# Kernel tuning notes

Hardware: AMD Instinct MI355X
Metric: run time of the kernel (lower is better)

The kernel has to match this reference:

```python
import jax, jax.numpy as jnp
import numpy as np

B, L, D_FEAT = 16, 2048, 512
H, D_HID, UNITS = 8, 512, 512


def setup_inputs() -> dict:
    key = jax.random.key(0)
    ks = jax.random.split(key, 8)
    s_feat = 1.0 / np.sqrt(D_FEAT)
    s_hid = 1.0 / np.sqrt(D_HID)
    s_u = 1.0 / np.sqrt(UNITS)
    return {
        "features": jax.random.normal(ks[0], (B, L, D_FEAT), jnp.float32),
        "hidden": jax.random.normal(ks[1], (B, H, D_HID), jnp.float32),
        # Per-head Dense params stacked along a leading head axis.
        "W1": jax.random.normal(ks[2], (H, D_FEAT, UNITS), jnp.float32) * s_feat,
        "b1": jnp.zeros((H, UNITS), jnp.float32),
        "W2": jax.random.normal(ks[3], (H, D_HID, UNITS), jnp.float32) * s_hid,
        "b2": jnp.zeros((H, UNITS), jnp.float32),
        "V": jax.random.normal(ks[4], (H, UNITS), jnp.float32) * s_u,
        "bV": jnp.zeros((H,), jnp.float32),
    }


def reference(features, hidden, W1, b1, W2, b2, V, bV):
    # features: [B, L, Df]; hidden: [B, H, Dh]
    # Per-head: tanh(W1(features) + W2(hidden_h)) -> V -> softmax over L -> weighted sum.
    f_proj = jnp.einsum("bld,hdu->bhlu", features, W1) + b1[None, :, None, :]   # [B,H,L,U]
    h_proj = jnp.einsum("bhd,hdu->bhu", hidden, W2) + b2[None, :, :]            # [B,H,U]
    act = jnp.tanh(f_proj + h_proj[:, :, None, :])                               # [B,H,L,U]
    score = jnp.einsum("bhlu,hu->bhl", act, V) + bV[None, :, None]               # [B,H,L]
    attn = jax.nn.softmax(score, axis=-1)                                        # softmax over L
    context = jnp.einsum("bhl,bld->bhd", attn, features)                         # [B,H,Df]
    # Original stacks weights (each [B,L,1]) along axis=2 -> [B,L,H,1]
    attention_weights = jnp.transpose(attn, (0, 2, 1))[..., None]                # [B,L,H,1]
    return context, attention_weights
```

## Files before the change

kernel.cpp:

```cpp
#include <hip/hip_runtime.h>
#include <hip/hip_bf16.h>

#define B_ 16
#define L_ 2048
#define DF 512
#define H_ 8
#define DH 512
#define U_ 512

typedef unsigned short u16;
typedef __attribute__((ext_vector_type(8))) short bf16x8;
typedef __attribute__((ext_vector_type(4))) float f32x4;

__device__ __forceinline__ u16 f2bf(float x) {
  __hip_bfloat16 h = __float2bfloat16(x);
  u16 u;
  __builtin_memcpy(&u, &h, 2);
  return u;
}

__device__ __forceinline__ float bf2f(u16 u) {
  unsigned x = ((unsigned)u) << 16;
  float f;
  __builtin_memcpy(&f, &x, 4);
  return f;
}

__device__ __forceinline__ void load_lds16(const void* g, void* l) {
  __builtin_amdgcn_global_load_lds(
      (const __attribute__((address_space(1))) void*)g,
      (__attribute__((address_space(3))) void*)l, 16, 0, 0);
}

__device__ __forceinline__ float fast_tanh2(float x) {
  float e = __expf(2.f * x);
  return 1.f - __fdividef(2.f, e + 1.f);
}

__global__ __launch_bounds__(256) void prep_kernel(
    const float* __restrict__ F, u16* __restrict__ Abf,
    const float* __restrict__ W1, u16* __restrict__ W1T,
    const float* __restrict__ hidden, const float* __restrict__ W2,
    float* __restrict__ hpart) {
  __shared__ float t[32][33];
  __shared__ float hs[B_][64];
  if (blockIdx.x < 16384) {
    size_t i = ((size_t)blockIdx.x * 256 + threadIdx.x) * 4;
    float4 v = *(const float4*)(F + i);
    ushort4 o;
    o.x = f2bf(v.x); o.y = f2bf(v.y); o.z = f2bf(v.z); o.w = f2bf(v.w);
    *(ushort4*)(Abf + i) = o;
  } else if (blockIdx.x < 18432) {
    int bid = blockIdx.x - 16384;
    int d0 = (bid & 15) * 32, u0 = ((bid >> 4) & 15) * 32, h = bid >> 8;
    const float* src = W1 + (size_t)h * DF * U_;
    u16* dst = W1T + (size_t)h * U_ * DF;
#pragma unroll
    for (int i = 0; i < 4; ++i) {
      int idx = threadIdx.x + i * 256;
      int r = idx >> 5, c = idx & 31;
      t[r][c] = src[(size_t)(d0 + r) * U_ + u0 + c];
    }
    __syncthreads();
#pragma unroll
    for (int i = 0; i < 4; ++i) {
      int idx = threadIdx.x + i * 256;
      int r = idx >> 5, c = idx & 31;
      dst[(size_t)(u0 + r) * DF + d0 + c] = f2bf(t[c][r]);
    }
  } else {
    int bid = blockIdx.x - 18432;
    int h = bid & 7, uy = (bid >> 3) & 1, dz = bid >> 4;
    int u = uy * 256 + threadIdx.x;
    int d0 = dz * 64;
    for (int idx = threadIdx.x; idx < B_ * 64; idx += 256) {
      int b = idx >> 6, d = idx & 63;
      hs[b][d] = hidden[(size_t)(b * H_ + h) * DH + d0 + d];
    }
    __syncthreads();
    float acc[B_];
#pragma unroll
    for (int b = 0; b < B_; b++) acc[b] = 0.f;
    const float* w2p = W2 + ((size_t)h * DH + d0) * U_ + u;
    for (int d = 0; d < 64; d++) {
      float w = w2p[(size_t)d * U_];
#pragma unroll
      for (int b = 0; b < B_; b++) acc[b] += hs[b][d] * w;
    }
#pragma unroll
    for (int b = 0; b < B_; b++)
      hpart[(((size_t)dz * B_ + b) * H_ + h) * U_ + u] = acc[b];
  }
}

__global__ __launch_bounds__(256) void hproj_combine_kernel(
    const float* __restrict__ partial, const float* __restrict__ b1,
    const float* __restrict__ b2, float* __restrict__ c) {
  int i = blockIdx.x * 256 + threadIdx.x;
  int hu = i & (H_ * U_ - 1);
  float s = b1[hu] + b2[hu];
#pragma unroll
  for (int z = 0; z < 8; z++) s += partial[(size_t)z * B_ * H_ * U_ + i];
  c[i] = s;
}

#define BKV 64

__global__ __launch_bounds__(1024, 4) void score_kernel(
    const u16* __restrict__ Abf, const u16* __restrict__ W1T,
    const float* __restrict__ C, const float* __restrict__ V,
    float* __restrict__ score) {
  int l0 = blockIdx.x * 256;
  int b = blockIdx.y, h = blockIdx.z;
  int tid = threadIdx.x;
  int lane = tid & 63, wid = tid >> 6;
  int wr = wid >> 2, wc = wid & 3;
  int rl = lane & 15, q = lane >> 4;
  int khalf = q << 3;

  __shared__ u16 As[2][256 * BKV];
  __shared__ u16 Bs[2][256 * BKV];
  __shared__ float redsm[4][256];

  const u16* Fb = Abf + ((size_t)b * L_ + l0) * DF;
  const u16* Wh = W1T + (size_t)h * U_ * DF;
  const float* Cb = C + (size_t)(b * H_ + h) * U_;
  const float* Vh = V + (size_t)h * U_;

  float cu[2][4], vv[2][4];
#pragma unroll
  for (int nc = 0; nc < 2; ++nc)
#pragma unroll
    for (int n = 0; n < 4; ++n) {
      int col = nc * 256 + wc * 64 + n * 16 + rl;
      cu[nc][n] = Cb[col];
      vv[nc][n] = Vh[col];
    }

  float part[16];
#pragma unroll
  for (int p = 0; p < 16; ++p) part[p] = 0.f;

  f32x4 acc[4][4];
#pragma unroll
  for (int m = 0; m < 4; ++m)
#pragma unroll
    for (int n = 0; n < 4; ++n)
#pragma unroll
      for (int j = 0; j < 4; ++j) acc[m][n][j] = cu[0][n];

#define STAGE(buf, kb, N0)                                                 \
  {                                                                        \
    _Pragma("unroll") for (int i_ = 0; i_ < 2; ++i_) {                     \
      int idx_ = i_ * 1024 + tid;                                          \
      int row_ = idx_ >> 3;                                                \
      int ke_ = ((idx_ & 7) ^ (row_ & 7)) << 3;                            \
      load_lds16(Fb + ((size_t)row_ << 9) + (kb) + ke_,                    \
                 &As[buf][idx_ * 8]);                                      \
      load_lds16(Wh + (((size_t)((N0) + row_)) << 9) + (kb) + ke_,         \
                 &Bs[buf][idx_ * 8]);                                      \
    }                                                                      \
  }

#define COMPUTE(bufi)                                                      \
  {                                                                        \
    _Pragma("unroll") for (int ss = 0; ss < 2; ++ss) {                     \
      bf16x8 bF[4];                                                        \
      _Pragma("unroll") for (int n = 0; n < 4; ++n) {                      \
        int rB = wc * 64 + n * 16 + rl;                                    \
        bF[n] = *(const bf16x8*)&Bs[bufi][(rB << 6) +                      \
                                          ((ss * 32 + khalf) ^             \
                                           ((rB & 7) << 3))];              \
      }                                                                    \
      _Pragma("unroll") for (int m = 0; m < 4; ++m) {                      \
        int rA = wr * 64 + m * 16 + rl;                                    \
        bf16x8 aF = *(const bf16x8*)&As[bufi][(rA << 6) +                  \
                                             ((ss * 32 + khalf) ^          \
                                              ((rA & 7) << 3))];           \
        _Pragma("unroll") for (int n = 0; n < 4; ++n)                      \
          acc[m][n] = __builtin_amdgcn_mfma_f32_16x16x32_bf16(             \
              aF, bF[n], acc[m][n], 0, 0, 0);                              \
      }                                                                    \
    }                                                                      \
  }

  STAGE(0, 0, 0);

#pragma unroll 1
  for (int s = 0; s < 16; ++s) {
    int cur = s & 1;
    if (s < 15) {
      int kb = ((s + 1) & 7) * BKV;
      int N0n = ((s + 1) >> 3) * 256;
      STAGE(cur ^ 1, kb, N0n);
      asm volatile("s_waitcnt vmcnt(4)" ::: "memory");
    } else {
      asm volatile("s_waitcnt vmcnt(0)" ::: "memory");
    }
    __builtin_amdgcn_s_barrier();
    COMPUTE(cur);
    if (s == 7) {
#pragma unroll
      for (int n = 0; n < 4; ++n)
#pragma unroll
        for (int m = 0; m < 4; ++m)
#pragma unroll
          for (int j = 0; j < 4; ++j) {
            part[m * 4 + j] += fast_tanh2(acc[m][n][j]) * vv[0][n];
            acc[m][n][j] = cu[1][n];
          }
    }
    asm volatile("s_waitcnt lgkmcnt(0)" ::: "memory");
    __builtin_amdgcn_s_barrier();
  }
#pragma unroll
  for (int n = 0; n < 4; ++n)
#pragma unroll
    for (int m = 0; m < 4; ++m)
#pragma unroll
      for (int j = 0; j < 4; ++j)
        part[m * 4 + j] += fast_tanh2(acc[m][n][j]) * vv[1][n];
#undef STAGE
#undef COMPUTE

#pragma unroll
  for (int p = 0; p < 16; ++p) {
    float v = part[p];
    v += __shfl_xor(v, 1, 64);
    v += __shfl_xor(v, 2, 64);
    v += __shfl_xor(v, 4, 64);
    v += __shfl_xor(v, 8, 64);
    part[p] = v;
  }
  __syncthreads();
  if (rl == 0) {
#pragma unroll
    for (int m = 0; m < 4; ++m)
#pragma unroll
      for (int j = 0; j < 4; ++j)
        redsm[wc][wr * 64 + m * 16 + q * 4 + j] = part[m * 4 + j];
  }
  __syncthreads();
  if (tid < 256) {
    float s = redsm[0][tid] + redsm[1][tid] + redsm[2][tid] + redsm[3][tid];
    score[(size_t)(b * H_ + h) * L_ + l0 + tid] = s;
  }
}

__global__ __launch_bounds__(256) void softmax_kernel(
    const float* __restrict__ score, float* __restrict__ attn,
    float* __restrict__ aw_out) {
  int bh = blockIdx.x;
  int b = bh / H_, h = bh % H_;
  const float* s = score + (size_t)bh * L_;
  __shared__ float sv[L_];
  __shared__ float red[256];

  for (int i = threadIdx.x; i < L_ / 4; i += 256)
    ((float4*)sv)[i] = ((const float4*)s)[i];
  __syncthreads();

  float m = -1e30f;
  for (int l = threadIdx.x; l < L_; l += 256) m = fmaxf(m, sv[l]);
  red[threadIdx.x] = m;
  __syncthreads();
  for (int st = 128; st > 0; st >>= 1) {
    if (threadIdx.x < st)
      red[threadIdx.x] = fmaxf(red[threadIdx.x], red[threadIdx.x + st]);
    __syncthreads();
  }
  m = red[0];
  __syncthreads();

  float sum = 0.f;
  for (int l = threadIdx.x; l < L_; l += 256) sum += __expf(sv[l] - m);
  red[threadIdx.x] = sum;
  __syncthreads();
  for (int st = 128; st > 0; st >>= 1) {
    if (threadIdx.x < st) red[threadIdx.x] += red[threadIdx.x + st];
    __syncthreads();
  }
  float inv = 1.f / red[0];

  for (int l = threadIdx.x; l < L_; l += 256) {
    float a = __expf(sv[l] - m) * inv;
    attn[(size_t)bh * L_ + l] = a;
    aw_out[((size_t)b * L_ + l) * H_ + h] = a;
  }
}

__global__ __launch_bounds__(256) void context_part_kernel(
    const u16* __restrict__ Abf, const float* __restrict__ attn,
    float* __restrict__ partial) {
  int b = blockIdx.x;
  int d0 = blockIdx.y * 64;
  int lz = blockIdx.z;
  int td = threadIdx.x & 63;
  int tl = threadIdx.x >> 6;

  __shared__ float as[H_][256];
  for (int idx = threadIdx.x; idx < H_ * 256; idx += 256)
    as[idx >> 8][idx & 255] =
        attn[((size_t)b * H_ + (idx >> 8)) * L_ + lz * 256 + (idx & 255)];
  __syncthreads();

  float acc[H_] = {};
  for (int l = tl; l < 256; l += 4) {
    float f = bf2f(Abf[((size_t)b * L_ + lz * 256 + l) * DF + d0 + td]);
#pragma unroll
    for (int h = 0; h < H_; h++) acc[h] += as[h][l] * f;
  }

  __shared__ float red[4][H_][64];
#pragma unroll
  for (int h = 0; h < H_; h++) red[tl][h][td] = acc[h];
  __syncthreads();
  if (tl == 0) {
#pragma unroll
    for (int h = 0; h < H_; h++) {
      float v = red[0][h][td] + red[1][h][td] + red[2][h][td] + red[3][h][td];
      partial[(size_t)lz * B_ * H_ * DF + ((size_t)b * H_ + h) * DF + d0 + td] =
          v;
    }
  }
}

__global__ __launch_bounds__(256) void context_combine_kernel(
    const float* __restrict__ partial, float* __restrict__ ctx_out) {
  int i = blockIdx.x * 256 + threadIdx.x;
  float s = 0.f;
#pragma unroll
  for (int z = 0; z < 8; z++) s += partial[(size_t)z * B_ * H_ * DF + i];
  ctx_out[i] = s;
}

extern "C" void kernel_launch(void* const* d_in, const int* in_sizes, int n_in,
                              void* d_out, int out_size, void* d_ws,
                              size_t ws_size, hipStream_t stream) {
  const float* features = (const float*)d_in[0];
  const float* hidden   = (const float*)d_in[1];
  const float* W1       = (const float*)d_in[2];
  const float* b1       = (const float*)d_in[3];
  const float* W2       = (const float*)d_in[4];
  const float* b2       = (const float*)d_in[5];
  const float* V        = (const float*)d_in[6];

  float* out = (float*)d_out;
  float* ctx_out = out;
  float* aw_out  = out + B_ * H_ * DF;

  float* c_buf = (float*)d_ws;
  float* score = c_buf + (size_t)B_ * H_ * U_;
  float* attn  = score;
  float* hpart = score;
  float* cpart = score + (size_t)B_ * H_ * L_;
  u16* Abf = (u16*)(cpart + (size_t)8 * B_ * H_ * DF);
  u16* W1T = Abf + (size_t)B_ * L_ * DF;

  prep_kernel<<<16384 + 2048 + 128, 256, 0, stream>>>(features, Abf, W1, W1T,
                                                      hidden, W2, hpart);
  hproj_combine_kernel<<<(B_ * H_ * U_) / 256, 256, 0, stream>>>(hpart, b1, b2,
                                                                 c_buf);
  score_kernel<<<dim3(L_ / 256, B_, H_), 1024, 0, stream>>>(Abf, W1T, c_buf, V,
                                                            score);
  softmax_kernel<<<B_ * H_, 256, 0, stream>>>(score, attn, aw_out);
  context_part_kernel<<<dim3(B_, DF / 64, 8), 256, 0, stream>>>(Abf, attn,
                                                                cpart);
  context_combine_kernel<<<(B_ * H_ * DF) / 256, 256, 0, stream>>>(cpart,
                                                                   ctx_out);
}
```

Before: 267.5 us.

## Shrink score GEMM tile to 128 rows with 32-wide K steps

The score kernel now uses 512-thread blocks covering 128 sequence rows instead of 1024 threads covering 256, with K staged in 32-element slices and a matching 4-way XOR swizzle. The two 256-column U chunks are processed in an outer loop, each with its own 16-step double-buffered pipeline, and C/V values are loaded per chunk. This cuts LDS use per block and doubles the grid, aiming for better occupancy and latency hiding. In exchange, W1 tiles are reloaded twice as often per output row, and the pipeline drains and refills at each chunk boundary.

```diff
diff --git a/kernel.cpp b/kernel.cpp
--- a/kernel.cpp
+++ b/kernel.cpp
@@ -104,122 +104,111 @@
   c[i] = s;
 }
 
-#define BKV 64
-
-__global__ __launch_bounds__(1024, 4) void score_kernel(
+#define BKW 32
+
+__global__ __launch_bounds__(512, 4) void score_kernel(
     const u16* __restrict__ Abf, const u16* __restrict__ W1T,
     const float* __restrict__ C, const float* __restrict__ V,
     float* __restrict__ score) {
-  int l0 = blockIdx.x * 256;
+  int l0 = blockIdx.x * 128;
   int b = blockIdx.y, h = blockIdx.z;
   int tid = threadIdx.x;
   int lane = tid & 63, wid = tid >> 6;
   int wr = wid >> 2, wc = wid & 3;
   int rl = lane & 15, q = lane >> 4;
-  int khalf = q << 3;
-
-  __shared__ u16 As[2][256 * BKV];
-  __shared__ u16 Bs[2][256 * BKV];
-  __shared__ float redsm[4][256];
+
+  __shared__ u16 As[2][128 * BKW];
+  __shared__ u16 Bs[2][256 * BKW];
+  __shared__ float redsm[4][128];
 
   const u16* Fb = Abf + ((size_t)b * L_ + l0) * DF;
   const u16* Wh = W1T + (size_t)h * U_ * DF;
   const float* Cb = C + (size_t)(b * H_ + h) * U_;
   const float* Vh = V + (size_t)h * U_;
 
-  float cu[2][4], vv[2][4];
-#pragma unroll
-  for (int nc = 0; nc < 2; ++nc)
-#pragma unroll
-    for (int n = 0; n < 4; ++n) {
-      int col = nc * 256 + wc * 64 + n * 16 + rl;
-      cu[nc][n] = Cb[col];
-      vv[nc][n] = Vh[col];
-    }
-
   float part[16];
 #pragma unroll
   for (int p = 0; p < 16; ++p) part[p] = 0.f;
 
-  f32x4 acc[4][4];
-#pragma unroll
-  for (int m = 0; m < 4; ++m)
-#pragma unroll
-    for (int n = 0; n < 4; ++n)
-#pragma unroll
-      for (int j = 0; j < 4; ++j) acc[m][n][j] = cu[0][n];
-
-#define STAGE(buf, kb, N0)                                                 \
+#define STAGE(buf, kb, ubase)                                              \
   {                                                                        \
+    {                                                                      \
+      int row_ = tid >> 2;                                                 \
+      int ke_ = ((tid & 3) ^ ((row_ >> 1) & 3)) << 3;                      \
+      load_lds16(Fb + ((size_t)row_ << 9) + (kb) + ke_,                    \
+                 &As[buf][tid * 8]);                                       \
+    }                                                                      \
     _Pragma("unroll") for (int i_ = 0; i_ < 2; ++i_) {                     \
-      int idx_ = i_ * 1024 + tid;                                          \
-      int row_ = idx_ >> 3;                                                \
-      int ke_ = ((idx_ & 7) ^ (row_ & 7)) << 3;                            \
-      load_lds16(Fb + ((size_t)row_ << 9) + (kb) + ke_,                    \
-                 &As[buf][idx_ * 8]);                                      \
-      load_lds16(Wh + (((size_t)((N0) + row_)) << 9) + (kb) + ke_,         \
+      int idx_ = i_ * 512 + tid;                                           \
+      int row_ = idx_ >> 2;                                                \
+      int ke_ = ((idx_ & 3) ^ ((row_ >> 1) & 3)) << 3;                     \
+      load_lds16(Wh + (((size_t)((ubase) + row_)) << 9) + (kb) + ke_,      \
                  &Bs[buf][idx_ * 8]);                                      \
     }                                                                      \
   }
 
 #define COMPUTE(bufi)                                                      \
   {                                                                        \
-    _Pragma("unroll") for (int ss = 0; ss < 2; ++ss) {                     \
-      bf16x8 bF[4];                                                        \
-      _Pragma("unroll") for (int n = 0; n < 4; ++n) {                      \
-        int rB = wc * 64 + n * 16 + rl;                                    \
-        bF[n] = *(const bf16x8*)&Bs[bufi][(rB << 6) +                      \
-                                          ((ss * 32 + khalf) ^             \
-                                           ((rB & 7) << 3))];              \
-      }                                                                    \
-      _Pragma("unroll") for (int m = 0; m < 4; ++m) {                      \
-        int rA = wr * 64 + m * 16 + rl;                                    \
-        bf16x8 aF = *(const bf16x8*)&As[bufi][(rA << 6) +                  \
-                                             ((ss * 32 + khalf) ^          \
-                                              ((rA & 7) << 3))];           \
-        _Pragma("unroll") for (int n = 0; n < 4; ++n)                      \
-          acc[m][n] = __builtin_amdgcn_mfma_f32_16x16x32_bf16(             \
-              aF, bF[n], acc[m][n], 0, 0, 0);                              \
-      }                                                                    \
+    bf16x8 bF[4];                                                          \
+    _Pragma("unroll") for (int n = 0; n < 4; ++n) {                        \
+      int rB = wc * 64 + n * 16 + rl;                                      \
+      bF[n] = *(const bf16x8*)&Bs[bufi][(rB << 5) +                        \
+                                        ((q ^ ((rB >> 1) & 3)) << 3)];     \
     }                                                                      \
-  }
-
-  STAGE(0, 0, 0);
+    _Pragma("unroll") for (int m = 0; m < 4; ++m) {                        \
+      int rA = wr * 64 + m * 16 + rl;                                      \
+      bf16x8 aF = *(const bf16x8*)&As[bufi][(rA << 5) +                    \
+                                           ((q ^ ((rA >> 1) & 3)) << 3)];  \
+      _Pragma("unroll") for (int n = 0; n < 4; ++n)                        \
+        acc[m][n] = __builtin_amdgcn_mfma_f32_16x16x32_bf16(               \
+            aF, bF[n], acc[m][n], 0, 0, 0);                                \
+    }                                                                      \
+  }
 
 #pragma unroll 1
-  for (int s = 0; s < 16; ++s) {
-    int cur = s & 1;
-    if (s < 15) {
-      int kb = ((s + 1) & 7) * BKV;
-      int N0n = ((s + 1) >> 3) * 256;
-      STAGE(cur ^ 1, kb, N0n);
-      asm volatile("s_waitcnt vmcnt(4)" ::: "memory");
-    } else {
-      asm volatile("s_waitcnt vmcnt(0)" ::: "memory");
-    }
-    __builtin_amdgcn_s_barrier();
-    COMPUTE(cur);
-    if (s == 7) {
+  for (int nc = 0; nc < 2; ++nc) {
+    int ubase = nc * 256;
+    float cu[4], vv[4];
+#pragma unroll
+    for (int n = 0; n < 4; ++n) {
+      int col = ubase + wc * 64 + n * 16 + rl;
+      cu[n] = Cb[col];
+      vv[n] = Vh[col];
+    }
+    f32x4 acc[4][4];
+#pragma unroll
+    for (int m = 0; m < 4; ++m)
 #pragma unroll
       for (int n = 0; n < 4; ++n)
 #pragma unroll
-        for (int m = 0; m < 4; ++m)
-#pragma unroll
-          for (int j = 0; j < 4; ++j) {
-            part[m * 4 + j] += fast_tanh2(acc[m][n][j]) * vv[0][n];
-            acc[m][n][j] = cu[1][n];
-          }
-    }
-    asm volatile("s_waitcnt lgkmcnt(0)" ::: "memory");
-    __builtin_amdgcn_s_barrier();
-  }
-#pragma unroll
-  for (int n = 0; n < 4; ++n)
-#pragma unroll
-    for (int m = 0; m < 4; ++m)
-#pragma unroll
-      for (int j = 0; j < 4; ++j)
-        part[m * 4 + j] += fast_tanh2(acc[m][n][j]) * vv[1][n];
+        for (int j = 0; j < 4; ++j) acc[m][n][j] = cu[n];
+
+    asm volatile("s_waitcnt vmcnt(0)" ::: "memory");
+    STAGE(0, 0, ubase);
+
+#pragma unroll 1
+    for (int t = 0; t < 16; ++t) {
+      int cur = t & 1;
+      if (t < 15) {
+        STAGE(cur ^ 1, (t + 1) * BKW, ubase);
+        asm volatile("s_waitcnt vmcnt(3)" ::: "memory");
+      } else {
+        asm volatile("s_waitcnt vmcnt(0)" ::: "memory");
+      }
+      __builtin_amdgcn_s_barrier();
+      COMPUTE(cur);
+      asm volatile("s_waitcnt lgkmcnt(0)" ::: "memory");
+      __builtin_amdgcn_s_barrier();
+    }
+
+#pragma unroll
+    for (int n = 0; n < 4; ++n)
+#pragma unroll
+      for (int m = 0; m < 4; ++m)
+#pragma unroll
+        for (int j = 0; j < 4; ++j)
+          part[m * 4 + j] += fast_tanh2(acc[m][n][j]) * vv[n];
+  }
 #undef STAGE
 #undef COMPUTE
 
@@ -241,7 +230,7 @@
         redsm[wc][wr * 64 + m * 16 + q * 4 + j] = part[m * 4 + j];
   }
   __syncthreads();
-  if (tid < 256) {
+  if (tid < 128) {
     float s = redsm[0][tid] + redsm[1][tid] + redsm[2][tid] + redsm[3][tid];
     score[(size_t)(b * H_ + h) * L_ + l0 + tid] = s;
   }
@@ -361,8 +350,8 @@
                                                       hidden, W2, hpart);
   hproj_combine_kernel<<<(B_ * H_ * U_) / 256, 256, 0, stream>>>(hpart, b1, b2,
                                                                  c_buf);
-  score_kernel<<<dim3(L_ / 256, B_, H_), 1024, 0, stream>>>(Abf, W1T, c_buf, V,
-                                                            score);
+  score_kernel<<<dim3(L_ / 128, B_, H_), 512, 0, stream>>>(Abf, W1T, c_buf, V,
+                                                           score);
   softmax_kernel<<<B_ * H_, 256, 0, stream>>>(score, attn, aw_out);
   context_part_kernel<<<dim3(B_, DF / 64, 8), 256, 0, stream>>>(Abf, attn,
                                                                 cpart);
```

Result: faster. 251.0 us (-6.2%).
